# Optimization experiments

Measured on AMD Instinct MI355X. Metric: run time of the kernel, lower is better.

## Reference

```python
import jax, jax.numpy as jnp
import numpy as np

RADIUS = 12
SIGMA = 5.0
T0 = 0.1
TOP_PERCENT = 0.1
CURVE_STEPS = 8


def _gaussian_kernel():
    xs = jnp.arange(-RADIUS, RADIUS + 1, dtype=jnp.float32)
    k = jnp.exp(-0.5 * jnp.square(xs / SIGMA))
    k = k / jnp.sum(k)
    k2 = k[:, None] * k[None, :]
    # depthwise kernel (O=3, I/group=1, 25, 25)
    return jnp.tile(k2[None, None], (3, 1, 1, 1))


def tanh01(x):
    return (jnp.tanh(x) + 1) / 2


def tanh_range(l, r):
    return lambda x: tanh01(x) * (r - l) + l


def _parse_params(p):
    omega = tanh_range(0.1, 1.0)(p[:, 0:1])                          # (B,1)
    wb_mask = jnp.array([0.0, 1.0, 1.0], dtype=p.dtype)[None]
    wb = jnp.exp(tanh_range(-0.5, 0.5)(p[:, 1:4] * wb_mask))         # (B,3)
    lg = jnp.log(jnp.asarray(3.0, dtype=p.dtype))
    gamma = jnp.exp(tanh_range(-lg, lg)(p[:, 4:5]))                  # (B,1)
    tone = tanh_range(0.5, 2.0)(p[:, 5:13].reshape(-1, 1, 8)[:, None, None, :])  # (B,1,1,1,8)
    contrast = jnp.tanh(p[:, 13:14])                                 # (B,1)
    sharpen = tanh_range(0.0, 5.0)(p[:, 14:15])                      # (B,1)
    return omega, wb, gamma, tone, contrast, sharpen


def _apply_defog(x, omega):
    # mirror `if x.min() < 0: x = (x+1)/2` in a jit-safe way
    x = jnp.where(jnp.min(x) < 0, (x + 1) / 2, x)
    B, C, H, W = x.shape
    dark = jnp.min(x, axis=1)                                        # (B,H,W)
    k = int(H * W * TOP_PERCENT)
    flat = dark.reshape(B, H * W)
    _, idx = jax.lax.top_k(flat, k)                                  # (B,k)
    xf = x.reshape(B, C, H * W)
    sel = jnp.take_along_axis(xf, idx[:, None, :], axis=2)           # (B,C,k)
    A = jnp.max(sel, axis=2)[:, :, None, None]                       # (B,C,1,1)
    t = jnp.clip(1 - omega[:, :, None] * dark, T0, 1.0)[:, None]     # (B,1,H,W)
    J = (x - A) / t + A
    return jnp.clip(J, 0.0, 1.0)


def _apply_white_balance(image, wb):
    denom = (0.27 * wb[:, 0] + 0.67 * wb[:, 1] + 0.06 * wb[:, 2] + 1e-05)[:, None]
    p = wb / denom
    return image * p[:, :, None, None]


def _apply_gamma(image, gamma):
    g = jnp.tile(gamma, (1, 3))[:, :, None, None]                    # (B,3,1,1)
    return jnp.power(jnp.maximum(image, 1e-4), g)


def _apply_tone(image, tone):
    tone_sum = jnp.sum(tone, axis=-1) + 1e-30                        # (B,1,1,1)
    total = jnp.zeros_like(image)
    for i in range(CURVE_STEPS):
        total = total + jnp.clip(image - 1.0 * i / CURVE_STEPS, 0.0, 1.0 / CURVE_STEPS) * tone[:, :, :, :, i]
    return total * CURVE_STEPS / tone_sum


def _apply_contrast(image, contrast):
    # faithful to source: rgb2lum indexes the LAST axis (W), giving (B,3,H,1)
    lum = (0.27 * image[:, :, :, 0] + 0.67 * image[:, :, :, 1] + 0.06 * image[:, :, :, 2])[:, :, :, None]
    lum = jnp.clip(lum, 0.0, 1.0)
    contrast_lum = -jnp.cos(jnp.pi * lum) * 0.5 + 0.5
    contrast_image = image / (lum + 1e-6) * contrast_lum
    c = contrast[:, :, None, None]                                   # (B,1,1,1)
    return (1 - c) * image + c * contrast_image


def _apply_sharpen(image, sharpen):
    kernel = _gaussian_kernel()
    blurred = jax.lax.conv_general_dilated(
        image, kernel, window_strides=(1, 1),
        padding=[(RADIUS, RADIUS), (RADIUS, RADIUS)],
        dimension_numbers=('NCHW', 'OIHW', 'NCHW'),
        feature_group_count=3)
    s = sharpen[:, None, None, :]                                    # (B,1,1,1)
    return (image - blurred) * s + image


def setup_inputs() -> dict:
    key = jax.random.key(0)
    k1, k2 = jax.random.split(key)
    x = jax.random.uniform(k1, (16, 3, 512, 512), dtype=jnp.float32)
    params = jax.random.normal(k2, (16, 15), dtype=jnp.float32)
    return {"x": x, "params": params}


def reference(x, params):
    omega, wb, gamma, tone, contrast, sharpen = _parse_params(params)
    image = _apply_defog(x, omega)
    image = _apply_white_balance(image, wb)
    image = _apply_gamma(image, gamma)
    image = _apply_tone(image, tone)
    image = _apply_contrast(image, contrast)
    image = _apply_sharpen(image, sharpen)
    return jax.nn.sigmoid(image)
```

## Files before the change

kernel.cpp:

```cpp
#include <hip/hip_runtime.h>
#include <math.h>

#define NB 16
#define NC 3
#define NH 512
#define NW 512
#define NHW (NH*NW)
#define KSEL 26214u
#define PI_F 3.14159265358979f
#define LOG2E_F 1.44269504f
#define POISON_U32 0xAAAAAAAAu

typedef _Float16 half4v __attribute__((ext_vector_type(4)));
typedef _Float16 half8v __attribute__((ext_vector_type(8)));
typedef float    float4v __attribute__((ext_vector_type(4)));

#define TMPH_OFF   0
#define PCH_OFF    (NB*NC*NHW/2)
#define HIST_OFF   (PCH_OFF + NB*NC*NHW/2)
#define BMAX_OFF   (HIST_OFF + NB*256)
#define AVAL_OFF   (BMAX_OFF + NB*768)
#define PBUF_OFF   (AVAL_OFF + NB*3)
#define GW_OFF     (PBUF_OFF + NB*32)

__device__ __forceinline__ float fast_rcp(float x)  { return __builtin_amdgcn_rcpf(x); }
__device__ __forceinline__ float fast_exp2(float x) { return __builtin_amdgcn_exp2f(x); }
__device__ __forceinline__ float fast_log2(float x) { return __builtin_amdgcn_logf(x); }

__device__ __forceinline__ int swzf4(int f) {
  return (f & ~7) | ((3*f + (f >> 3)) & 7);
}

__device__ __forceinline__ float chain_tt(float xv, float dv, float omega, float Aval,
                                          float wbp, float g, const float* tone) {
  float t = fminf(fmaxf(1.f - omega*dv, 0.1f), 1.f);
  float J = (xv - Aval)*fast_rcp(t) + Aval;
  J = fminf(fmaxf(J, 0.f), 1.f);
  float v = J * wbp;
  float u = fast_exp2(g * fast_log2(fmaxf(v, 1e-4f)));
  float tt = 0.f;
#pragma unroll
  for (int i = 0; i < 8; i++)
    tt = fmaf(fminf(fmaxf(u - 0.125f*(float)i, 0.f), 0.125f), tone[i], tt);
  return tt;
}

__global__ __launch_bounds__(256) void k_stats(const float* __restrict__ x,
                                               unsigned* __restrict__ hist,
                                               unsigned* __restrict__ binmax) {
  __shared__ unsigned lh[8*256];
  __shared__ unsigned lbm[8][768];
  int tid = threadIdx.x, b = blockIdx.y;
  for (int i = tid; i < 8*256; i += 256) lh[i] = 0u;
  for (int i = tid; i < 8*768; i += 256) ((unsigned*)lbm)[i] = 0u;
  __syncthreads();
  const float4* x0 = (const float4*)(x + (size_t)b*NC*NHW);
  const float4* x1 = x0 + NHW/4;
  const float4* x2 = x1 + NHW/4;
  unsigned* lhm = lh + (tid & 7)*256;
  unsigned* bmr = lbm[tid & 7];
  int base = blockIdx.x*1024 + tid;
#pragma unroll
  for (int it = 0; it < 4; it++) {
    int i = base + it*256;
    float4 a = x0[i], g = x1[i], r = x2[i];
    float dv[4] = { fminf(fminf(a.x,g.x),r.x), fminf(fminf(a.y,g.y),r.y),
                    fminf(fminf(a.z,g.z),r.z), fminf(fminf(a.w,g.w),r.w) };
    float av[4] = {a.x,a.y,a.z,a.w}, gv[4] = {g.x,g.y,g.z,g.w}, rv[4] = {r.x,r.y,r.z,r.w};
#pragma unroll
    for (int q = 0; q < 4; q++) {
      unsigned bin = __float_as_uint(dv[q]) >> 24;
      atomicAdd(&lhm[bin], 1u);
      atomicMax(&bmr[bin],       __float_as_uint(av[q]));
      atomicMax(&bmr[256 + bin], __float_as_uint(gv[q]));
      atomicMax(&bmr[512 + bin], __float_as_uint(rv[q]));
    }
  }
  __syncthreads();
  {
    unsigned s = 0;
    for (int r2 = 0; r2 < 8; r2++) s += lh[r2*256 + tid];
    if (s) atomicAdd(&hist[b*256 + tid], s);
  }
  for (int idx = tid; idx < 768; idx += 256) {
    unsigned m = lbm[0][idx];
#pragma unroll
    for (int r2 = 1; r2 < 8; r2++) m = max(m, lbm[r2][idx]);
    if (m) atomicMin(&binmax[b*768 + idx], 0x7FFFFFFFu - m);
  }
}

__global__ void k_scan(const unsigned* __restrict__ hist,
                       const unsigned* __restrict__ binmax,
                       float* __restrict__ avals,
                       const float* __restrict__ p, float* __restrict__ pbuf,
                       float* __restrict__ gw) {
  int b = blockIdx.x, tid = threadIdx.x;
  if (tid < 64) {
    int lane = tid;
    unsigned cnt[4], s = 0;
#pragma unroll
    for (int j = 0; j < 4; j++) {
      cnt[j] = hist[b*256 + (255 - (lane*4+j))] - POISON_U32;
      s += cnt[j];
    }
    unsigned inc = s;
    for (int off = 1; off < 64; off <<= 1) {
      unsigned n = __shfl_up(inc, off);
      if (lane >= off) inc += n;
    }
    unsigned excl = inc - s;
    bool found = (excl < KSEL && KSEL <= inc);
    int localBin = 0;
    if (found) {
      unsigned run = excl; int binj = 0;
#pragma unroll
      for (int j = 0; j < 4; j++) {
        unsigned nb = run + cnt[j];
        if (KSEL > run && KSEL <= nb) binj = j;
        run = nb;
      }
      localBin = 255 - (lane*4 + binj);
    }
    unsigned long long mask = __ballot(found ? 1 : 0);
    int src = (int)__ffsll((long long)mask) - 1;
    int bstar = __shfl(localBin, src);
#pragma unroll
    for (int c = 0; c < 3; c++) {
      float m = 0.f;
#pragma unroll
      for (int j = 0; j < 4; j++) {
        int bin = 255 - (lane*4 + j);
        if (bin >= bstar) {
          unsigned enc = binmax[b*768 + c*256 + bin];
          unsigned bits = (enc <= 0x7FFFFFFFu) ? (0x7FFFFFFFu - enc) : 0u;
          m = fmaxf(m, __uint_as_float(bits));
        }
      }
      for (int off = 1; off < 64; off <<= 1) m = fmaxf(m, __shfl_xor(m, off));
      if (lane == 0) avals[b*3 + c] = m;
    }
  } else if (tid == 64) {
    const float* pp = p + b*15;
    float* ob = pbuf + b*32;
    float omega = (tanhf(pp[0])+1.f)*0.5f*0.9f + 0.1f;
    float wb0 = 1.0f;
    float wb1 = expf((tanhf(pp[2])+1.f)*0.5f - 0.5f);
    float wb2 = expf((tanhf(pp[3])+1.f)*0.5f - 0.5f);
    float denom = 0.27f*wb0 + 0.67f*wb1 + 0.06f*wb2 + 1e-5f;
    float lg = logf(3.0f);
    float g = expf((tanhf(pp[4])+1.f)*0.5f*(2.f*lg) - lg);
    float ts = 0.f, tone[8];
    for (int i = 0; i < 8; i++) { tone[i] = (tanhf(pp[5+i])+1.f)*0.5f*1.5f + 0.5f; ts += tone[i]; }
    ts += 1e-30f;
    ob[0] = omega; ob[1] = wb0/denom; ob[2] = wb1/denom; ob[3] = wb2/denom; ob[4] = g;
    for (int i = 0; i < 8; i++) ob[5+i] = tone[i];
    ob[13] = 8.0f/ts;
    ob[14] = tanhf(pp[13]);
    ob[15] = (tanhf(pp[14])+1.f)*0.5f*5.0f;
  } else if (tid == 65 && b == 0) {
    float wv[25], wsum = 0.f;
    for (int i = 0; i < 25; i++) { float d = (float)(i-12)/5.0f; wv[i] = expf(-0.5f*d*d); wsum += wv[i]; }
    for (int i = 0; i < 25; i++) gw[i] = wv[i]/wsum;
  }
}

__global__ __launch_bounds__(256) void k_hblur(
    const float* __restrict__ x, const float* __restrict__ pbuf,
    const float* __restrict__ avals, const float* __restrict__ gw,
    _Float16* __restrict__ tmph, _Float16* __restrict__ pch) {
  __shared__ __align__(16) float pcp[3][4][544];
  int tid = threadIdx.x;
  int row = tid >> 6, lane = tid & 63;
  int b = blockIdx.y;
  int h = blockIdx.x*4 + row;
  const float* pb = pbuf + b*32;
  float omega = pb[0], g = pb[4], ts = pb[13], cc = pb[14];
  float wbp[3] = {pb[1], pb[2], pb[3]};
  float tone[8];
#pragma unroll
  for (int i = 0; i < 8; i++) tone[i] = pb[5+i];
  float Av[3] = {avals[b*3], avals[b*3+1], avals[b*3+2]};
  if (lane < 4) {
    float4 z; z.x = 0.f; z.y = 0.f; z.z = 0.f; z.w = 0.f;
    int fa = swzf4(lane)*4, fb = swzf4(132 + lane)*4;
#pragma unroll
    for (int c = 0; c < 3; c++) {
      *(float4*)(&pcp[c][row][0] + fa) = z;
      *(float4*)(&pcp[c][row][0] + fb) = z;
    }
  }
  const float4* xr0 = (const float4*)(x + ((size_t)b*3 + 0)*NHW + (size_t)h*NW);
  const float4* xr1 = (const float4*)(x + ((size_t)b*3 + 1)*NHW + (size_t)h*NW);
  const float4* xr2 = (const float4*)(x + ((size_t)b*3 + 2)*NHW + (size_t)h*NW);
  float s00=0.f,s01=0.f,s02=0.f,s10=0.f,s11=0.f,s12=0.f,s20=0.f,s21=0.f,s22=0.f;
#pragma unroll
  for (int m = 0; m < 2; m++) {
    int i4 = lane + m*64;
    float4 v0 = xr0[i4], v1 = xr1[i4], v2 = xr2[i4];
    float4 d;
    d.x = fminf(fminf(v0.x,v1.x),v2.x); d.y = fminf(fminf(v0.y,v1.y),v2.y);
    d.z = fminf(fminf(v0.z,v1.z),v2.z); d.w = fminf(fminf(v0.w,v1.w),v2.w);
    float4 p0, p1, p2;
    p0.x = chain_tt(v0.x, d.x, omega, Av[0], wbp[0], g, tone);
    p0.y = chain_tt(v0.y, d.y, omega, Av[0], wbp[0], g, tone);
    p0.z = chain_tt(v0.z, d.z, omega, Av[0], wbp[0], g, tone);
    p0.w = chain_tt(v0.w, d.w, omega, Av[0], wbp[0], g, tone);
    p1.x = chain_tt(v1.x, d.x, omega, Av[1], wbp[1], g, tone);
    p1.y = chain_tt(v1.y, d.y, omega, Av[1], wbp[1], g, tone);
    p1.z = chain_tt(v1.z, d.z, omega, Av[1], wbp[1], g, tone);
    p1.w = chain_tt(v1.w, d.w, omega, Av[1], wbp[1], g, tone);
    p2.x = chain_tt(v2.x, d.x, omega, Av[2], wbp[2], g, tone);
    p2.y = chain_tt(v2.y, d.y, omega, Av[2], wbp[2], g, tone);
    p2.z = chain_tt(v2.z, d.z, omega, Av[2], wbp[2], g, tone);
    p2.w = chain_tt(v2.w, d.w, omega, Av[2], wbp[2], g, tone);
    if (m == 0) {
      s00 = p0.x; s01 = p0.y; s02 = p0.z;
      s10 = p1.x; s11 = p1.y; s12 = p1.z;
      s20 = p2.x; s21 = p2.y; s22 = p2.z;
    }
    int fw = swzf4(4 + i4)*4;
    *(float4*)(&pcp[0][row][0] + fw) = p0;
    *(float4*)(&pcp[1][row][0] + fw) = p1;
    *(float4*)(&pcp[2][row][0] + fw) = p2;
  }
  __syncthreads();
  float rf0, rf1, rf2;
  {
    float t0 = 0.f, t1 = 0.f, t2 = 0.f;
    if (lane == 0) {
      float l0 = fminf(fmaxf((0.27f*s00 + 0.67f*s01 + 0.06f*s02)*ts, 0.f), 1.f);
      float l1 = fminf(fmaxf((0.27f*s10 + 0.67f*s11 + 0.06f*s12)*ts, 0.f), 1.f);
      float l2 = fminf(fmaxf((0.27f*s20 + 0.67f*s21 + 0.06f*s22)*ts, 0.f), 1.f);
      t0 = ts*((1.f - cc) + cc*(0.5f - 0.5f*__cosf(PI_F*l0))*fast_rcp(l0 + 1e-6f));
      t1 = ts*((1.f - cc) + cc*(0.5f - 0.5f*__cosf(PI_F*l1))*fast_rcp(l1 + 1e-6f));
      t2 = ts*((1.f - cc) + cc*(0.5f - 0.5f*__cosf(PI_F*l2))*fast_rcp(l2 + 1e-6f));
    }
    rf0 = __shfl(t0, 0); rf1 = __shfl(t1, 0); rf2 = __shfl(t2, 0);
  }
  float kw[25];
#pragma unroll
  for (int j = 0; j < 25; j++) kw[j] = gw[j];
  int fidx[8];
#pragma unroll
  for (int r = 0; r < 8; r++) fidx[r] = swzf4(2*lane + 1 + r)*4;
  float rfa[3] = {rf0, rf1, rf2};
#pragma unroll
  for (int c = 0; c < 3; c++) {
    float rfv = rfa[c];
    const float* rp = &pcp[c][row][0];
    float4 w[8];
#pragma unroll
    for (int r = 0; r < 8; r++) w[r] = *(const float4*)(rp + fidx[r]);
    float acc[8] = {0,0,0,0,0,0,0,0};
#pragma unroll
    for (int r = 0; r < 8; r++) {
      float vs[4] = {w[r].x, w[r].y, w[r].z, w[r].w};
#pragma unroll
      for (int q = 0; q < 4; q++) {
        int idx = r*4 + q;
#pragma unroll
        for (int i = 0; i < 8; i++) {
          int j = idx - i;
          if (j >= 0 && j < 25) acc[i] = fmaf(kw[j], vs[q], acc[i]);
        }
      }
    }
    size_t off = ((size_t)b*3 + c)*NHW + (size_t)h*NW + lane*8;
    half8v th;
#pragma unroll
    for (int i = 0; i < 8; i++) th[i] = (_Float16)(acc[i]*rfv);
    *(half8v*)(tmph + off) = th;
    half8v ph;
    ph[0] = (_Float16)(w[3].x*rfv); ph[1] = (_Float16)(w[3].y*rfv);
    ph[2] = (_Float16)(w[3].z*rfv); ph[3] = (_Float16)(w[3].w*rfv);
    ph[4] = (_Float16)(w[4].x*rfv); ph[5] = (_Float16)(w[4].y*rfv);
    ph[6] = (_Float16)(w[4].z*rfv); ph[7] = (_Float16)(w[4].w*rfv);
    *(half8v*)(pch + off) = ph;
  }
}

__global__ __launch_bounds__(256) void k_vblur(
    const _Float16* __restrict__ tmph, const _Float16* __restrict__ pch,
    const float* __restrict__ pbuf, const float* __restrict__ gw,
    float* __restrict__ out) {
  __shared__ _Float16 sh[152*64];
  int tid = threadIdx.x;
  int bc = blockIdx.z, b = bc/3;
  int w0 = blockIdx.x*64, h0 = blockIdx.y*128;
  const _Float16* tr = tmph + (size_t)bc*NHW;
  for (int idx = tid; idx < 152*8; idx += 256) {
    int r = idx >> 3, seg = idx & 7;
    int gh = h0 - 12 + r;
    uint4 v = make_uint4(0u,0u,0u,0u);
    if (gh >= 0 && gh < NH) v = *(const uint4*)(tr + (size_t)gh*NW + w0 + seg*8);
    *(uint4*)&sh[r*64 + seg*8] = v;
  }
  __syncthreads();
  float kw[25];
#pragma unroll
  for (int j = 0; j < 25; j++) kw[j] = gw[j];
  int wq = tid & 15, rg = tid >> 4;
  int rowbase = rg*8;
  float4v acc[8];
#pragma unroll
  for (int i = 0; i < 8; i++) acc[i] = (float4v)0.f;
#pragma unroll
  for (int r = 0; r < 32; r++) {
    half4v hv = *(const half4v*)&sh[(rowbase + r)*64 + wq*4];
    float4v v = __builtin_convertvector(hv, float4v);
#pragma unroll
    for (int i = 0; i < 8; i++) {
      int j = r - i;
      if (j >= 0 && j < 25) acc[i] += kw[j]*v;
    }
  }
  float sharp = pbuf[b*32 + 15];
#pragma unroll
  for (int i = 0; i < 8; i++) {
    int h = h0 + rowbase + i;
    size_t off = (size_t)bc*NHW + (size_t)h*NW + w0 + wq*4;
    half4v pcv = *(const half4v*)(pch + off);
    float4v pc = __builtin_convertvector(pcv, float4v);
    float4v res = (pc - acc[i])*sharp + pc;
    float4v o;
    o.x = fast_rcp(1.f + fast_exp2(-res.x*LOG2E_F));
    o.y = fast_rcp(1.f + fast_exp2(-res.y*LOG2E_F));
    o.z = fast_rcp(1.f + fast_exp2(-res.z*LOG2E_F));
    o.w = fast_rcp(1.f + fast_exp2(-res.w*LOG2E_F));
    *(float4v*)(out + off) = o;
  }
}

extern "C" void kernel_launch(void* const* d_in, const int* in_sizes, int n_in,
                              void* d_out, int out_size, void* d_ws, size_t ws_size,
                              hipStream_t stream) {
  const float* x = (const float*)d_in[0];
  const float* params = (const float*)d_in[1];
  float* out = (float*)d_out;
  float* ws = (float*)d_ws;

  _Float16* tmph = (_Float16*)(ws + TMPH_OFF);
  _Float16* pch  = (_Float16*)(ws + PCH_OFF);
  unsigned* hist   = (unsigned*)(ws + HIST_OFF);
  unsigned* binmax = (unsigned*)(ws + BMAX_OFF);
  float* avals = ws + AVAL_OFF;
  float* pbuf  = ws + PBUF_OFF;
  float* gw    = ws + GW_OFF;

  k_stats<<<dim3(64, NB), 256, 0, stream>>>(x, hist, binmax);
  k_scan<<<NB, 128, 0, stream>>>(hist, binmax, avals, params, pbuf, gw);
  k_hblur<<<dim3(NH/4, NB), 256, 0, stream>>>(x, pbuf, avals, gw, tmph, pch);
  k_vblur<<<dim3(NW/64, NH/128, NB*NC), 256, 0, stream>>>(tmph, pch, pbuf, gw, out);
}
```

Baseline: 145.7 us.

## Process channels sequentially in hblur with double-buffered LDS and new swizzle

The horizontal blur kernel now computes the per-pixel chain one channel at a time into a two-slot LDS ring buffer instead of staging all three channels up front. Channels 1 and 2 are re-read from global memory, and only the dark-channel minimum and channel 0 are kept in registers. The change cuts LDS use from three to two channel buffers and lowers register pressure, which may raise occupancy. It also replaces the float4 LDS swizzle function. The cost is an extra barrier per channel and repeated global loads of channels 1 and 2. The single-buffer-per-parity reuse also looks like it could race without a barrier before the slot is overwritten.

Result: no change. 147.8 us (+1.4%).

```diff
diff --git a/kernel.cpp b/kernel.cpp
--- a/kernel.cpp
+++ b/kernel.cpp
@@ -28,7 +28,9 @@
 __device__ __forceinline__ float fast_log2(float x) { return __builtin_amdgcn_logf(x); }
 
 __device__ __forceinline__ int swzf4(int f) {
-  return (f & ~7) | ((3*f + (f >> 3)) & 7);
+  int t = f & 7;
+  int g = ((f >> 3) & 1) ? ((3 - t) & 7) : t;
+  return (f & ~7) | g;
 }
 
 __device__ __forceinline__ float chain_tt(float xv, float dv, float omega, float Aval,
@@ -43,6 +45,16 @@
   for (int i = 0; i < 8; i++)
     tt = fmaf(fminf(fmaxf(u - 0.125f*(float)i, 0.f), 0.125f), tone[i], tt);
   return tt;
+}
+
+__device__ __forceinline__ float4 chain4(float4 v, float4 d, float omega, float A,
+                                         float wbp, float g, const float* tone) {
+  float4 r;
+  r.x = chain_tt(v.x, d.x, omega, A, wbp, g, tone);
+  r.y = chain_tt(v.y, d.y, omega, A, wbp, g, tone);
+  r.z = chain_tt(v.z, d.z, omega, A, wbp, g, tone);
+  r.w = chain_tt(v.w, d.w, omega, A, wbp, g, tone);
+  return r;
 }
 
 __global__ __launch_bounds__(256) void k_stats(const float* __restrict__ x,
@@ -169,7 +181,7 @@
     const float* __restrict__ x, const float* __restrict__ pbuf,
     const float* __restrict__ avals, const float* __restrict__ gw,
     _Float16* __restrict__ tmph, _Float16* __restrict__ pch) {
-  __shared__ __align__(16) float pcp[3][4][544];
+  __shared__ __align__(16) float pcp[2][4][544];
   int tid = threadIdx.x;
   int row = tid >> 6, lane = tid & 63;
   int b = blockIdx.y;
@@ -185,73 +197,65 @@
     float4 z; z.x = 0.f; z.y = 0.f; z.z = 0.f; z.w = 0.f;
     int fa = swzf4(lane)*4, fb = swzf4(132 + lane)*4;
 #pragma unroll
-    for (int c = 0; c < 3; c++) {
-      *(float4*)(&pcp[c][row][0] + fa) = z;
-      *(float4*)(&pcp[c][row][0] + fb) = z;
-    }
-  }
-  const float4* xr0 = (const float4*)(x + ((size_t)b*3 + 0)*NHW + (size_t)h*NW);
-  const float4* xr1 = (const float4*)(x + ((size_t)b*3 + 1)*NHW + (size_t)h*NW);
-  const float4* xr2 = (const float4*)(x + ((size_t)b*3 + 2)*NHW + (size_t)h*NW);
-  float s00=0.f,s01=0.f,s02=0.f,s10=0.f,s11=0.f,s12=0.f,s20=0.f,s21=0.f,s22=0.f;
-#pragma unroll
-  for (int m = 0; m < 2; m++) {
-    int i4 = lane + m*64;
-    float4 v0 = xr0[i4], v1 = xr1[i4], v2 = xr2[i4];
-    float4 d;
-    d.x = fminf(fminf(v0.x,v1.x),v2.x); d.y = fminf(fminf(v0.y,v1.y),v2.y);
-    d.z = fminf(fminf(v0.z,v1.z),v2.z); d.w = fminf(fminf(v0.w,v1.w),v2.w);
-    float4 p0, p1, p2;
-    p0.x = chain_tt(v0.x, d.x, omega, Av[0], wbp[0], g, tone);
-    p0.y = chain_tt(v0.y, d.y, omega, Av[0], wbp[0], g, tone);
-    p0.z = chain_tt(v0.z, d.z, omega, Av[0], wbp[0], g, tone);
-    p0.w = chain_tt(v0.w, d.w, omega, Av[0], wbp[0], g, tone);
-    p1.x = chain_tt(v1.x, d.x, omega, Av[1], wbp[1], g, tone);
-    p1.y = chain_tt(v1.y, d.y, omega, Av[1], wbp[1], g, tone);
-    p1.z = chain_tt(v1.z, d.z, omega, Av[1], wbp[1], g, tone);
-    p1.w = chain_tt(v1.w, d.w, omega, Av[1], wbp[1], g, tone);
-    p2.x = chain_tt(v2.x, d.x, omega, Av[2], wbp[2], g, tone);
-    p2.y = chain_tt(v2.y, d.y, omega, Av[2], wbp[2], g, tone);
-    p2.z = chain_tt(v2.z, d.z, omega, Av[2], wbp[2], g, tone);
-    p2.w = chain_tt(v2.w, d.w, omega, Av[2], wbp[2], g, tone);
-    if (m == 0) {
-      s00 = p0.x; s01 = p0.y; s02 = p0.z;
-      s10 = p1.x; s11 = p1.y; s12 = p1.z;
-      s20 = p2.x; s21 = p2.y; s22 = p2.z;
-    }
-    int fw = swzf4(4 + i4)*4;
-    *(float4*)(&pcp[0][row][0] + fw) = p0;
-    *(float4*)(&pcp[1][row][0] + fw) = p1;
-    *(float4*)(&pcp[2][row][0] + fw) = p2;
-  }
-  __syncthreads();
-  float rf0, rf1, rf2;
+    for (int bu = 0; bu < 2; bu++) {
+      *(float4*)(&pcp[bu][row][0] + fa) = z;
+      *(float4*)(&pcp[bu][row][0] + fb) = z;
+    }
+  }
+  const float* xbase = x + (size_t)b*3*NHW + (size_t)h*NW;
+  float4 va[2], d4[2];
   {
-    float t0 = 0.f, t1 = 0.f, t2 = 0.f;
-    if (lane == 0) {
-      float l0 = fminf(fmaxf((0.27f*s00 + 0.67f*s01 + 0.06f*s02)*ts, 0.f), 1.f);
-      float l1 = fminf(fmaxf((0.27f*s10 + 0.67f*s11 + 0.06f*s12)*ts, 0.f), 1.f);
-      float l2 = fminf(fmaxf((0.27f*s20 + 0.67f*s21 + 0.06f*s22)*ts, 0.f), 1.f);
-      t0 = ts*((1.f - cc) + cc*(0.5f - 0.5f*__cosf(PI_F*l0))*fast_rcp(l0 + 1e-6f));
-      t1 = ts*((1.f - cc) + cc*(0.5f - 0.5f*__cosf(PI_F*l1))*fast_rcp(l1 + 1e-6f));
-      t2 = ts*((1.f - cc) + cc*(0.5f - 0.5f*__cosf(PI_F*l2))*fast_rcp(l2 + 1e-6f));
-    }
-    rf0 = __shfl(t0, 0); rf1 = __shfl(t1, 0); rf2 = __shfl(t2, 0);
+    const float4* xr0 = (const float4*)(xbase);
+    const float4* xr1 = (const float4*)(xbase + NHW);
+    const float4* xr2 = (const float4*)(xbase + 2*(size_t)NHW);
+#pragma unroll
+    for (int m = 0; m < 2; m++) {
+      int i4 = lane + m*64;
+      float4 v0 = xr0[i4], v1 = xr1[i4], v2 = xr2[i4];
+      d4[m].x = fminf(fminf(v0.x,v1.x),v2.x);
+      d4[m].y = fminf(fminf(v0.y,v1.y),v2.y);
+      d4[m].z = fminf(fminf(v0.z,v1.z),v2.z);
+      d4[m].w = fminf(fminf(v0.w,v1.w),v2.w);
+      va[m] = v0;
+    }
   }
   float kw[25];
 #pragma unroll
   for (int j = 0; j < 25; j++) kw[j] = gw[j];
+  int fw0 = swzf4(4 + lane)*4, fw1 = swzf4(68 + lane)*4;
   int fidx[8];
 #pragma unroll
   for (int r = 0; r < 8; r++) fidx[r] = swzf4(2*lane + 1 + r)*4;
-  float rfa[3] = {rf0, rf1, rf2};
+
 #pragma unroll
   for (int c = 0; c < 3; c++) {
-    float rfv = rfa[c];
-    const float* rp = &pcp[c][row][0];
+    float4 p0, p1;
+    if (c == 0) {
+      p0 = chain4(va[0], d4[0], omega, Av[0], wbp[0], g, tone);
+      p1 = chain4(va[1], d4[1], omega, Av[0], wbp[0], g, tone);
+    } else {
+      const float4* xr = (const float4*)(xbase + (size_t)c*NHW);
+      asm volatile("" : "+v"(xr));
+      float4 u0 = xr[lane], u1 = xr[lane + 64];
+      p0 = chain4(u0, d4[0], omega, Av[c], wbp[c], g, tone);
+      p1 = chain4(u1, d4[1], omega, Av[c], wbp[c], g, tone);
+    }
+    float* bp = &pcp[c & 1][row][0];
+    *(float4*)(bp + fw0) = p0;
+    *(float4*)(bp + fw1) = p1;
+    __syncthreads();
+    float rf;
+    {
+      float t0 = 0.f;
+      if (lane == 0) {
+        float l = fminf(fmaxf((0.27f*p0.x + 0.67f*p0.y + 0.06f*p0.z)*ts, 0.f), 1.f);
+        t0 = ts*((1.f - cc) + cc*(0.5f - 0.5f*__cosf(PI_F*l))*fast_rcp(l + 1e-6f));
+      }
+      rf = __shfl(t0, 0);
+    }
     float4 w[8];
 #pragma unroll
-    for (int r = 0; r < 8; r++) w[r] = *(const float4*)(rp + fidx[r]);
+    for (int r = 0; r < 8; r++) w[r] = *(const float4*)(bp + fidx[r]);
     float acc[8] = {0,0,0,0,0,0,0,0};
 #pragma unroll
     for (int r = 0; r < 8; r++) {
@@ -269,13 +273,13 @@
     size_t off = ((size_t)b*3 + c)*NHW + (size_t)h*NW + lane*8;
     half8v th;
 #pragma unroll
-    for (int i = 0; i < 8; i++) th[i] = (_Float16)(acc[i]*rfv);
+    for (int i = 0; i < 8; i++) th[i] = (_Float16)(acc[i]*rf);
     *(half8v*)(tmph + off) = th;
     half8v ph;
-    ph[0] = (_Float16)(w[3].x*rfv); ph[1] = (_Float16)(w[3].y*rfv);
-    ph[2] = (_Float16)(w[3].z*rfv); ph[3] = (_Float16)(w[3].w*rfv);
-    ph[4] = (_Float16)(w[4].x*rfv); ph[5] = (_Float16)(w[4].y*rfv);
-    ph[6] = (_Float16)(w[4].z*rfv); ph[7] = (_Float16)(w[4].w*rfv);
+    ph[0] = (_Float16)(w[3].x*rf); ph[1] = (_Float16)(w[3].y*rf);
+    ph[2] = (_Float16)(w[3].z*rf); ph[3] = (_Float16)(w[3].w*rf);
+    ph[4] = (_Float16)(w[4].x*rf); ph[5] = (_Float16)(w[4].y*rf);
+    ph[6] = (_Float16)(w[4].z*rf); ph[7] = (_Float16)(w[4].w*rf);
     *(half8v*)(pch + off) = ph;
   }
 }
```
